# Optimization experiments

Hardware: AMD Instinct MI355X
Metric: run time of the kernel (lower is better)

Reference implementation:

```python
import jax, jax.numpy as jnp
import numpy as np

BIT = 4
HALF = 2 ** (BIT - 1)          # 8 -> signed integer grid [-8, 7]
N_LEVELS = 2 ** BIT - 1        # 15
COUT, CIN, KH, KW = 1024, 1024, 3, 3


def _flip_pass(r, err, up_num, up_err, up_pri, dn_num, dn_err, dn_pri):
    """One SQuant flip pass over rows (groups). Greedily flips the rounding
    direction of the highest-priority elements so each row's rounding-error
    sum becomes ~0, and hands off boundary priorities for the next pass
    (reconstruction of the SQuant_func CUDA kernel)."""
    G, K = r.shape
    rows = jnp.arange(G)
    e = err.sum(-1)                                    # (G,) error budget
    nflip = jnp.round(jnp.abs(e)).astype(jnp.int32)    # flips needed per row
    is_up = e < 0                                      # under-rounded -> flip up

    pri = jnp.where(is_up[:, None], up_pri, dn_pri)
    order = jnp.argsort(-pri, axis=-1)                 # descending priority
    rank = jnp.zeros((G, K), jnp.int32).at[rows[:, None], order].set(
        jnp.broadcast_to(jnp.arange(K, dtype=jnp.int32), (G, K)))
    flip = rank < nflip[:, None]

    cand_num = jnp.where(is_up[:, None], up_num, dn_num)
    cand_err = jnp.where(is_up[:, None], up_err, dn_err)
    new_r = jnp.where(flip, cand_num, r)
    new_err = jnp.where(flip, cand_err, err)

    # ---- boundary-priority handoff for the next (channel-wise) pass ----
    ni = jnp.take_along_axis(order, jnp.clip(nflip, 0, K - 1)[:, None], axis=-1)[:, 0]      # next candidate
    li = jnp.take_along_axis(order, jnp.clip(nflip - 1, 0, K - 1)[:, None], axis=-1)[:, 0]  # last flipped
    has_next = nflip < K
    has_last = nflip > 0
    next_pri = jnp.where(has_next, pri[rows, ni], 0.0)         # flip one more element
    last_pri = jnp.where(has_last, 1.0 - pri[rows, li], 0.0)   # revert the last flip

    z = jnp.zeros_like(pri)
    new_up_pri = z.at[rows, ni].add(jnp.where(is_up, next_pri, 0.0))
    new_up_pri = new_up_pri.at[rows, li].add(jnp.where(~is_up, last_pri, 0.0))
    new_dn_pri = z.at[rows, ni].add(jnp.where(~is_up, next_pri, 0.0))
    new_dn_pri = new_dn_pri.at[rows, li].add(jnp.where(is_up, last_pri, 0.0))

    # reverting the last flipped element restores its pre-flip value/error
    up_last = is_up & has_last
    dn_last = (~is_up) & has_last
    new_dn_num = dn_num.at[rows, li].set(jnp.where(up_last, r[rows, li], dn_num[rows, li]))
    new_dn_err = dn_err.at[rows, li].set(jnp.where(up_last, err[rows, li], dn_err[rows, li]))
    new_up_num = up_num.at[rows, li].set(jnp.where(dn_last, r[rows, li], up_num[rows, li]))
    new_up_err = up_err.at[rows, li].set(jnp.where(dn_last, err[rows, li], up_err[rows, li]))
    return new_r, new_err, new_up_num, new_up_err, new_up_pri, new_dn_num, new_dn_err, new_dn_pri


def _adaptive_round(q):
    t_min, t_max = float(-HALF), float(HALF - 1)
    r = jnp.round(q)
    err = r - q
    cand_up = (err < 0) & (q < t_max)    # elements that may be rounded up instead
    cand_dn = (err > 0) & (q > t_min)    # elements that may be rounded down instead
    up_num = jnp.where(cand_up, r + 1.0, r)
    up_err = jnp.where(cand_up, err + 1.0, 0.0)
    up_pri = jnp.where(cand_up, -err, 0.0)   # |rounding error|
    dn_num = jnp.where(cand_dn, r - 1.0, r)
    dn_err = jnp.where(cand_dn, err - 1.0, 0.0)
    dn_pri = jnp.where(cand_dn, err, 0.0)

    cout, cin = q.shape[0], q.shape[1]
    k = q.size // (cout * cin)
    st = tuple(a.reshape(cout * cin, k) for a in (r, err, up_num, up_err, up_pri, dn_num, dn_err, dn_pri))
    st = _flip_pass(*st)                               # SQuant-K: per (Cout,Cin) kernel
    st = tuple(a.reshape(cout, cin * k) for a in st)
    st = _flip_pass(*st)                               # SQuant-C: per output channel
    return st[0].reshape(q.shape)


def _squant_quantize(weight):
    flat = weight.reshape(weight.shape[0], -1)
    x_max = flat.max(1)
    x_min = flat.min(1)
    scale = N_LEVELS / jnp.maximum(x_max - x_min, 1e-8)   # asymmetric per-channel
    zp = jnp.round(scale * x_min) + HALF                  # signed, integral zero point
    bshape = (-1,) + (1,) * (weight.ndim - 1)
    scale = scale.reshape(bshape)
    zp = zp.reshape(bshape)
    q = scale * weight - zp                               # linear_quantize
    q = _adaptive_round(q)
    q = jnp.clip(q, -HALF, HALF - 1)
    return (q + zp) / scale                               # linear_dequantize


def setup_inputs() -> dict:
    key = jax.random.key(0)
    weight = jax.random.normal(key, (COUT, CIN, KH, KW), dtype=jnp.float32) * 0.05
    return {"weight": weight}


def reference(weight):
    return _squant_quantize(weight)
```

## Files before the change

### kernel.cpp

```cpp
#include <hip/hip_runtime.h>

#define NROW   1024
#define ROWLEN 9216
#define NGRP   1024
#define NT     256
#define GPT    4
#define LCAP   256

__device__ __forceinline__ int bucketOf(float v) {
    int b = (int)(v * 256.0f);
    return b > 255 ? 255 : b;
}
__device__ __forceinline__ int clip16(int v) { return v < -8 ? -8 : (v > 7 ? 7 : v); }

__device__ void replay_group(const float* wg, float scale, float zp,
                             float r[9], float err[9], float q[9],
                             int* nflip1, bool* isup1, int* li_out) {
    float pri[9];
    #pragma unroll
    for (int j = 0; j < 9; ++j) {
        float qq = __fsub_rn(__fmul_rn(scale, wg[j]), zp);
        float rr = rintf(qq);
        q[j] = qq; r[j] = rr; err[j] = __fsub_rn(rr, qq);
    }
    float e = __fadd_rn(
                __fadd_rn(__fadd_rn(__fadd_rn(err[0], err[1]), __fadd_rn(err[2], err[3])),
                          __fadd_rn(__fadd_rn(err[4], err[5]), __fadd_rn(err[6], err[7]))),
                err[8]);
    int nf0 = (int)rintf(fabsf(e));
    bool up = (e < 0.0f);
    #pragma unroll
    for (int j = 0; j < 9; ++j) {
        bool cand = up ? ((err[j] < 0.0f) && (q[j] < 7.0f))
                       : ((err[j] > 0.0f) && (q[j] > -8.0f));
        pri[j] = cand ? (up ? -err[j] : err[j]) : 0.0f;
    }
    int rank[9] = {0,0,0,0,0,0,0,0,0};
    #pragma unroll
    for (int a = 0; a < 9; ++a)
        #pragma unroll
        for (int b = a + 1; b < 9; ++b) {
            int c = (pri[a] >= pri[b]) ? 1 : 0;
            rank[b] += c; rank[a] += 1 - c;
        }
    int nf = nf0 < 9 ? nf0 : 9;
    int lip = nf - 1; if (lip < 0) lip = 0;
    int li = 0;
    #pragma unroll
    for (int j = 0; j < 9; ++j) if (rank[j] == lip) li = j;
    *nflip1 = nf0; *isup1 = up; *li_out = li;
}

__global__ __launch_bounds__(NT)
__attribute__((amdgpu_waves_per_eu(4, 4)))
void squant_kernel(const float* __restrict__ w, float* __restrict__ out) {
    __shared__ alignas(16) signed char s_r2[ROWLEN];
    __shared__ unsigned short s_upos[NGRP];
    __shared__ unsigned short s_dpos[NGRP];
    __shared__ float s_uval[NGRP];
    __shared__ float s_dval[NGRP];
    __shared__ signed char s_ucn[NGRP];
    __shared__ signed char s_dcn[NGRP];
    __shared__ float s_leaf[128];
    __shared__ int   s_hist[256];
    __shared__ float s_lv[LCAP];
    __shared__ unsigned short s_lg[LCAP];
    __shared__ float s_lut[16];
    __shared__ float s_wred[8];
    __shared__ float s_bc[2];
    __shared__ float s_e2s;
    __shared__ int   s_seli[2];
    __shared__ int   s_lcount;

    const int row = blockIdx.x;
    const int tid = threadIdx.x;
    const int lane = tid & 63, wid = tid >> 6;
    const float* wrow = w + (size_t)row * ROWLEN;

    float fe[36];
    float vmin =  3.402823466e38f;
    float vmax = -3.402823466e38f;
    const float4* wt4 = reinterpret_cast<const float4*>(wrow + 36 * tid);
    #pragma unroll
    for (int k = 0; k < 9; ++k) {
        float4 v = wt4[k];
        fe[4*k+0] = v.x; fe[4*k+1] = v.y; fe[4*k+2] = v.z; fe[4*k+3] = v.w;
        vmin = fminf(vmin, fminf(fminf(v.x, v.y), fminf(v.z, v.w)));
        vmax = fmaxf(vmax, fmaxf(fmaxf(v.x, v.y), fmaxf(v.z, v.w)));
    }
    #pragma unroll
    for (int o = 32; o > 0; o >>= 1) {
        vmin = fminf(vmin, __shfl_xor(vmin, o, 64));
        vmax = fmaxf(vmax, __shfl_xor(vmax, o, 64));
    }
    if (lane == 0) { s_wred[wid] = vmin; s_wred[4 + wid] = vmax; }
    __syncthreads();
    if (tid == 0) {
        float a = s_wred[0], b = s_wred[4];
        #pragma unroll
        for (int i = 1; i < 4; ++i) { a = fminf(a, s_wred[i]); b = fmaxf(b, s_wred[4 + i]); }
        s_bc[0] = a; s_bc[1] = b;
    }
    __syncthreads();
    const float scale = __fdiv_rn(15.0f, fmaxf(__fsub_rn(s_bc[1], s_bc[0]), 1e-8f));
    const float zp    = __fadd_rn(rintf(__fmul_rn(scale, s_bc[0])), 8.0f);
    if (tid < 16) s_lut[tid] = __fdiv_rn(__fadd_rn((float)(tid - 8), zp), scale);

    int pk[9] = {0,0,0,0,0,0,0,0,0};
    #pragma unroll
    for (int gi = 0; gi < GPT; ++gi) {
        const int g = tid * GPT + gi;
        const int base = g * 9;
        float r[9], err[9], pri[9];
        int cu_m = 0, cd_m = 0;
        #pragma unroll
        for (int j = 0; j < 9; ++j) {
            float wv = fe[9 * gi + j];
            float qq = __fsub_rn(__fmul_rn(scale, wv), zp);
            float rr = rintf(qq);
            float ee = __fsub_rn(rr, qq);
            r[j] = rr; err[j] = ee;
            if ((ee < 0.0f) && (qq <  7.0f)) cu_m |= (1 << j);
            if ((ee > 0.0f) && (qq > -8.0f)) cd_m |= (1 << j);
        }
        float e = __fadd_rn(
                    __fadd_rn(__fadd_rn(__fadd_rn(err[0], err[1]), __fadd_rn(err[2], err[3])),
                              __fadd_rn(__fadd_rn(err[4], err[5]), __fadd_rn(err[6], err[7]))),
                    err[8]);
        int nflip = (int)rintf(fabsf(e));
        const bool isup = (e < 0.0f);
        const float da = isup ? 1.0f : -1.0f;
        const int cm = isup ? cu_m : cd_m;
        #pragma unroll
        for (int j = 0; j < 9; ++j)
            pri[j] = ((cm >> j) & 1) ? fabsf(err[j]) : 0.0f;
        int rank[9] = {0,0,0,0,0,0,0,0,0};
        #pragma unroll
        for (int a = 0; a < 9; ++a)
            #pragma unroll
            for (int b = a + 1; b < 9; ++b) {
                int c = (pri[a] >= pri[b]) ? 1 : 0;
                rank[b] += c; rank[a] += 1 - c;
            }
        const int nf  = nflip < 9 ? nflip : 9;
        const int nip = nf < 8 ? nf : 8;
        int lip = nf - 1; if (lip < 0) lip = 0;

        int ni = 0, li = 0;
        float pri_ni = 0.0f, pri_li = 0.0f, r_ni = 0.0f, r_li = 0.0f;
        #pragma unroll
        for (int j = 0; j < 9; ++j) {
            bool cand = (cm >> j) & 1;
            bool flip = rank[j] < nf;
            float cnj = cand ? __fadd_rn(r[j], da) : r[j];
            float cej = cand ? __fadd_rn(err[j], da) : 0.0f;
            fe[9 * gi + j] = flip ? cej : err[j];
            int enc = clip16(__float2int_rn(flip ? cnj : r[j])) & 0xff;
            const int m = 9 * gi + j;
            pk[m >> 2] |= enc << (8 * (m & 3));
            if (rank[j] == nip) { ni = j; pri_ni = pri[j]; r_ni = r[j]; }
            if (rank[j] == lip) { li = j; pri_li = pri[j]; r_li = r[j]; }
        }
        const bool has_next = (nflip < 9);
        const bool has_last = (nflip > 0);
        const float next_pri = has_next ? pri_ni : 0.0f;
        const float last_pri = has_last ? __fsub_rn(1.0f, pri_li) : 0.0f;
        signed char ncv = (signed char)clip16(__float2int_rn(
            (pri_ni > 0.0f) ? __fadd_rn(r_ni, da) : r_ni));
        signed char lcv = (signed char)clip16(__float2int_rn(r_li));
        if (isup) {
            s_upos[g] = (unsigned short)(base + ni); s_uval[g] = next_pri; s_ucn[g] = ncv;
            s_dpos[g] = (unsigned short)(base + li); s_dval[g] = last_pri; s_dcn[g] = lcv;
        } else {
            s_dpos[g] = (unsigned short)(base + ni); s_dval[g] = next_pri; s_dcn[g] = ncv;
            s_upos[g] = (unsigned short)(base + li); s_uval[g] = last_pri; s_ucn[g] = lcv;
        }
    }
    {
        int* r2w = reinterpret_cast<int*>(s_r2);
        #pragma unroll
        for (int k = 0; k < 9; ++k) r2w[9 * tid + k] = pk[k];
    }

    {
        const int h = tid & 1;
        float pe[8];
        #pragma unroll
        for (int j = 0; j < 8; ++j) {
            float s = __fadd_rn(__fadd_rn(__fadd_rn(fe[j], fe[8 + j]), fe[16 + j]), fe[24 + j]);
            if (j < 4) s = __fadd_rn(s, fe[32 + j]);
            pe[j] = s;
        }
        #pragma unroll
        for (int j = 0; j < 8; ++j) pe[j] = __shfl_xor(pe[j], 1, 64);
        float po[8];
        #pragma unroll
        for (int j = 0; j < 4; ++j)
            po[j] = __fadd_rn(__fadd_rn(__fadd_rn(__fadd_rn(pe[j], fe[4 + j]),
                                                  fe[12 + j]), fe[20 + j]), fe[28 + j]);
        #pragma unroll
        for (int j = 4; j < 8; ++j)
            po[j] = __fadd_rn(__fadd_rn(__fadd_rn(__fadd_rn(__fadd_rn(pe[j], fe[j - 4]),
                                                  fe[4 + j]), fe[12 + j]), fe[20 + j]), fe[28 + j]);
        float res = __fadd_rn(__fadd_rn(__fadd_rn(po[0], po[1]), __fadd_rn(po[2], po[3])),
                              __fadd_rn(__fadd_rn(po[4], po[5]), __fadd_rn(po[6], po[7])));
        if (h) s_leaf[tid >> 1] = res;
        s_hist[tid] = 0;
        if (tid == 0) s_lcount = 0;
    }
    __syncthreads();
    if (tid < 64) {
        float v = __fadd_rn(s_leaf[2 * tid], s_leaf[2 * tid + 1]);
        #pragma unroll
        for (int o = 1; o < 64; o <<= 1) {
            float u = __shfl_xor(v, o, 64);
            v = __fadd_rn(v, u);
        }
        if (tid == 0) s_e2s = v;
    }
    __syncthreads();

    const float e2     = s_e2s;
    const int   nflip2 = (int)rintf(fabsf(e2));
    const bool  isup2  = (e2 < 0.0f);
    const float* val = isup2 ? s_uval : s_dval;
    const unsigned short* pos = isup2 ? s_upos : s_dpos;
    const signed char* cnv = isup2 ? s_ucn : s_dcn;

    int   gg[4]; float vv[4]; int bb[4];
    #pragma unroll
    for (int m = 0; m < 4; ++m) {
        gg[m] = tid + m * NT;
        vv[m] = val[gg[m]];
        bb[m] = (vv[m] > 0.0f) ? bucketOf(vv[m]) : -1;
        if (bb[m] >= 0) atomicAdd(&s_hist[bb[m]], 1);
    }
    __syncthreads();
    if (tid < 64) {
        int b0 = s_hist[4*tid], b1 = s_hist[4*tid+1], b2 = s_hist[4*tid+2], b3 = s_hist[4*tid+3];
        int s3 = b3, s2 = b2 + s3, s1 = b1 + s2, s0 = b0 + s1;
        int suf = s0;
        #pragma unroll
        for (int off = 1; off < 64; off <<= 1) {
            int o = __shfl_down(suf, off, 64);
            if (tid + off < 64) suf += o;
        }
        int above = suf - s0;
        s_hist[4*tid]   = s0 + above;
        s_hist[4*tid+1] = s1 + above;
        s_hist[4*tid+2] = s2 + above;
        s_hist[4*tid+3] = s3 + above;
    }
    __syncthreads();
    const int npos = s_hist[0];

    if (nflip2 > 0 && nflip2 <= npos) {
        {
            int Tb  = s_hist[tid];
            int Tb1 = (tid < 255) ? s_hist[tid + 1] : 0;
            if (Tb >= nflip2 && Tb1 < nflip2) { s_seli[0] = tid; s_seli[1] = nflip2 - Tb1; }
        }
        __syncthreads();
        const int B = s_seli[0], m = s_seli[1];
        #pragma unroll
        for (int mm = 0; mm < 4; ++mm) {
            if (bb[mm] > B) s_r2[pos[gg[mm]]] = cnv[gg[mm]];
            else if (bb[mm] == B) {
                int ix = atomicAdd(&s_lcount, 1);
                if (ix < LCAP) { s_lv[ix] = vv[mm]; s_lg[ix] = (unsigned short)gg[mm]; }
            }
        }
        __syncthreads();
        const int L = s_lcount;
        if (L <= LCAP) {
            #pragma unroll
            for (int mm = 0; mm < 4; ++mm) {
                if (bb[mm] != B) continue;
                int rk = 0;
                for (int l = 0; l < L; ++l) {
                    float lv = s_lv[l]; int lg = s_lg[l];
                    rk += (int)((lv > vv[mm]) || ((lv == vv[mm]) && (lg < gg[mm])));
                }
                if (rk < m) s_r2[pos[gg[mm]]] = cnv[gg[mm]];
            }
        } else {
            #pragma unroll
            for (int mm = 0; mm < 4; ++mm) {
                if (bb[mm] != B) continue;
                int rk = 0;
                for (int j = 0; j < NGRP; ++j) {
                    float vj = val[j];
                    if (vj > 0.0f && bucketOf(vj) == B)
                        rk += (int)((vj > vv[mm]) || ((vj == vv[mm]) && (j < gg[mm])));
                }
                if (rk < m) s_r2[pos[gg[mm]]] = cnv[gg[mm]];
            }
        }
    } else if (nflip2 > npos) {
        #pragma unroll
        for (int mm = 0; mm < 4; ++mm)
            if (bb[mm] >= 0) s_r2[pos[gg[mm]]] = cnv[gg[mm]];
        __syncthreads();
        if (tid == 0) {
            int c = 0; const int extra = nflip2 - npos;
            for (int g = 0; g < NGRP && c < extra; ++g) {
                float r[9], err[9], q[9]; int nf1; bool up1; int li;
                replay_group(wrow + 9 * g, scale, zp, r, err, q, &nf1, &up1, &li);
                for (int j = 0; j < 9 && c < extra; ++j) {
                    int p = 9 * g + j;
                    if (val[g] > 0.0f && pos[g] == p) continue;
                    float cnp;
                    if (isup2) { bool cu = (err[j] < 0.0f) && (q[j] < 7.0f);
                                 cnp = cu ? r[j] + 1.0f : r[j]; }
                    else       { bool cd = (err[j] > 0.0f) && (q[j] > -8.0f);
                                 cnp = cd ? r[j] - 1.0f : r[j]; }
                    if (nf1 > 0 && j == li && (up1 != isup2)) cnp = r[j];
                    s_r2[p] = (signed char)clip16(__float2int_rn(cnp));
                    ++c;
                }
            }
        }
    }
    __syncthreads();

    const int* r2i = reinterpret_cast<const int*>(s_r2);
    float4* o4 = reinterpret_cast<float4*>(out + (size_t)row * ROWLEN);
    #pragma unroll
    for (int k = 0; k < 9; ++k) {
        int i = tid + k * NT;
        int word = r2i[i];
        float4 o;
        o.x = s_lut[((int)(signed char)( word        & 0xff)) + 8];
        o.y = s_lut[((int)(signed char)((word >>  8) & 0xff)) + 8];
        o.z = s_lut[((int)(signed char)((word >> 16) & 0xff)) + 8];
        o.w = s_lut[((int)(signed char)((word >> 24) & 0xff)) + 8];
        o4[i] = o;
    }
}

extern "C" void kernel_launch(void* const* d_in, const int* in_sizes, int n_in,
                              void* d_out, int out_size, void* d_ws, size_t ws_size,
                              hipStream_t stream) {
    const float* w = (const float*)d_in[0];
    float* out = (float*)d_out;
    squant_kernel<<<dim3(NROW), dim3(NT), 0, stream>>>(w, out);
}
```

Before: 97.55 us.

## Double threads per row to 512 and reduce errors via shared memory

Raises the block size from 256 to 512 threads, so each thread handles 2 groups instead of 4 and holds fewer registers. The row error-sum reduction changes from a register/shuffle tree to writing per-element errors into a new 36 KB shared array and summing with 128 threads. This adds parallelism and latency hiding per row but costs more LDS per block and an extra shared round trip. The waves_per_eu(4,4) hint stays, so occupancy may now be limited by LDS.

```diff
diff --git a/kernel.cpp b/kernel.cpp
--- a/kernel.cpp
+++ b/kernel.cpp
@@ -3,8 +3,8 @@
 #define NROW   1024
 #define ROWLEN 9216
 #define NGRP   1024
-#define NT     256
-#define GPT    4
+#define NT     512
+#define GPT    2
 #define LCAP   256
 
 __device__ __forceinline__ int bucketOf(float v) {
@@ -55,6 +55,7 @@
 __attribute__((amdgpu_waves_per_eu(4, 4)))
 void squant_kernel(const float* __restrict__ w, float* __restrict__ out) {
     __shared__ alignas(16) signed char s_r2[ROWLEN];
+    __shared__ alignas(16) float s_err[ROWLEN];
     __shared__ unsigned short s_upos[NGRP];
     __shared__ unsigned short s_dpos[NGRP];
     __shared__ float s_uval[NGRP];
@@ -66,7 +67,7 @@
     __shared__ float s_lv[LCAP];
     __shared__ unsigned short s_lg[LCAP];
     __shared__ float s_lut[16];
-    __shared__ float s_wred[8];
+    __shared__ float s_wred[16];
     __shared__ float s_bc[2];
     __shared__ float s_e2s;
     __shared__ int   s_seli[2];
@@ -77,28 +78,28 @@
     const int lane = tid & 63, wid = tid >> 6;
     const float* wrow = w + (size_t)row * ROWLEN;
 
-    float fe[36];
+    float fe[18];
     float vmin =  3.402823466e38f;
     float vmax = -3.402823466e38f;
-    const float4* wt4 = reinterpret_cast<const float4*>(wrow + 36 * tid);
+    const float2* wt2 = reinterpret_cast<const float2*>(wrow + 18 * tid);
     #pragma unroll
     for (int k = 0; k < 9; ++k) {
-        float4 v = wt4[k];
-        fe[4*k+0] = v.x; fe[4*k+1] = v.y; fe[4*k+2] = v.z; fe[4*k+3] = v.w;
-        vmin = fminf(vmin, fminf(fminf(v.x, v.y), fminf(v.z, v.w)));
-        vmax = fmaxf(vmax, fmaxf(fmaxf(v.x, v.y), fmaxf(v.z, v.w)));
+        float2 v = wt2[k];
+        fe[2 * k] = v.x; fe[2 * k + 1] = v.y;
+        vmin = fminf(vmin, fminf(v.x, v.y));
+        vmax = fmaxf(vmax, fmaxf(v.x, v.y));
     }
     #pragma unroll
     for (int o = 32; o > 0; o >>= 1) {
         vmin = fminf(vmin, __shfl_xor(vmin, o, 64));
         vmax = fmaxf(vmax, __shfl_xor(vmax, o, 64));
     }
-    if (lane == 0) { s_wred[wid] = vmin; s_wred[4 + wid] = vmax; }
+    if (lane == 0) { s_wred[wid] = vmin; s_wred[8 + wid] = vmax; }
     __syncthreads();
     if (tid == 0) {
-        float a = s_wred[0], b = s_wred[4];
-        #pragma unroll
-        for (int i = 1; i < 4; ++i) { a = fminf(a, s_wred[i]); b = fmaxf(b, s_wred[4 + i]); }
+        float a = s_wred[0], b = s_wred[8];
+        #pragma unroll
+        for (int i = 1; i < 8; ++i) { a = fminf(a, s_wred[i]); b = fmaxf(b, s_wred[8 + i]); }
         s_bc[0] = a; s_bc[1] = b;
     }
     __syncthreads();
@@ -106,7 +107,7 @@
     const float zp    = __fadd_rn(rintf(__fmul_rn(scale, s_bc[0])), 8.0f);
     if (tid < 16) s_lut[tid] = __fdiv_rn(__fadd_rn((float)(tid - 8), zp), scale);
 
-    int pk[9] = {0,0,0,0,0,0,0,0,0};
+    int pk16[9] = {0,0,0,0,0,0,0,0,0};
     #pragma unroll
     for (int gi = 0; gi < GPT; ++gi) {
         const int g = tid * GPT + gi;
@@ -157,7 +158,7 @@
             fe[9 * gi + j] = flip ? cej : err[j];
             int enc = clip16(__float2int_rn(flip ? cnj : r[j])) & 0xff;
             const int m = 9 * gi + j;
-            pk[m >> 2] |= enc << (8 * (m & 3));
+            pk16[m >> 1] |= enc << (8 * (m & 1));
             if (rank[j] == nip) { ni = j; pri_ni = pri[j]; r_ni = r[j]; }
             if (rank[j] == lip) { li = j; pri_li = pri[j]; r_li = r[j]; }
         }
@@ -177,36 +178,32 @@
         }
     }
     {
-        int* r2w = reinterpret_cast<int*>(s_r2);
-        #pragma unroll
-        for (int k = 0; k < 9; ++k) r2w[9 * tid + k] = pk[k];
-    }
-
-    {
-        const int h = tid & 1;
-        float pe[8];
-        #pragma unroll
-        for (int j = 0; j < 8; ++j) {
-            float s = __fadd_rn(__fadd_rn(__fadd_rn(fe[j], fe[8 + j]), fe[16 + j]), fe[24 + j]);
-            if (j < 4) s = __fadd_rn(s, fe[32 + j]);
-            pe[j] = s;
-        }
-        #pragma unroll
-        for (int j = 0; j < 8; ++j) pe[j] = __shfl_xor(pe[j], 1, 64);
-        float po[8];
-        #pragma unroll
-        for (int j = 0; j < 4; ++j)
-            po[j] = __fadd_rn(__fadd_rn(__fadd_rn(__fadd_rn(pe[j], fe[4 + j]),
-                                                  fe[12 + j]), fe[20 + j]), fe[28 + j]);
-        #pragma unroll
-        for (int j = 4; j < 8; ++j)
-            po[j] = __fadd_rn(__fadd_rn(__fadd_rn(__fadd_rn(__fadd_rn(pe[j], fe[j - 4]),
-                                                  fe[4 + j]), fe[12 + j]), fe[20 + j]), fe[28 + j]);
-        float res = __fadd_rn(__fadd_rn(__fadd_rn(po[0], po[1]), __fadd_rn(po[2], po[3])),
-                              __fadd_rn(__fadd_rn(po[4], po[5]), __fadd_rn(po[6], po[7])));
-        if (h) s_leaf[tid >> 1] = res;
-        s_hist[tid] = 0;
-        if (tid == 0) s_lcount = 0;
+        short* r2s = reinterpret_cast<short*>(s_r2);
+        #pragma unroll
+        for (int k = 0; k < 9; ++k) r2s[9 * tid + k] = (short)pk16[k];
+        float2* se2 = reinterpret_cast<float2*>(s_err + 18 * tid);
+        #pragma unroll
+        for (int k = 0; k < 9; ++k) se2[k] = float2{fe[2 * k], fe[2 * k + 1]};
+    }
+    if (tid < 256) s_hist[tid] = 0;
+    if (tid == 0) s_lcount = 0;
+    __syncthreads();
+
+    if (tid < 128) {
+        const float4* q = reinterpret_cast<const float4*>(s_err + 72 * tid);
+        float4 A = q[0], B4 = q[1];
+        float a0 = A.x, a1 = A.y, a2 = A.z, a3 = A.w;
+        float a4 = B4.x, a5 = B4.y, a6 = B4.z, a7 = B4.w;
+        #pragma unroll
+        for (int i = 1; i < 9; ++i) {
+            float4 c = q[2 * i], d = q[2 * i + 1];
+            a0 = __fadd_rn(a0, c.x); a1 = __fadd_rn(a1, c.y);
+            a2 = __fadd_rn(a2, c.z); a3 = __fadd_rn(a3, c.w);
+            a4 = __fadd_rn(a4, d.x); a5 = __fadd_rn(a5, d.y);
+            a6 = __fadd_rn(a6, d.z); a7 = __fadd_rn(a7, d.w);
+        }
+        s_leaf[tid] = __fadd_rn(__fadd_rn(__fadd_rn(a0, a1), __fadd_rn(a2, a3)),
+                                __fadd_rn(__fadd_rn(a4, a5), __fadd_rn(a6, a7)));
     }
     __syncthreads();
     if (tid < 64) {
@@ -227,9 +224,9 @@
     const unsigned short* pos = isup2 ? s_upos : s_dpos;
     const signed char* cnv = isup2 ? s_ucn : s_dcn;
 
-    int   gg[4]; float vv[4]; int bb[4];
-    #pragma unroll
-    for (int m = 0; m < 4; ++m) {
+    int   gg[2]; float vv[2]; int bb[2];
+    #pragma unroll
+    for (int m = 0; m < 2; ++m) {
         gg[m] = tid + m * NT;
         vv[m] = val[gg[m]];
         bb[m] = (vv[m] > 0.0f) ? bucketOf(vv[m]) : -1;
@@ -255,7 +252,7 @@
     const int npos = s_hist[0];
 
     if (nflip2 > 0 && nflip2 <= npos) {
-        {
+        if (tid < 256) {
             int Tb  = s_hist[tid];
             int Tb1 = (tid < 255) ? s_hist[tid + 1] : 0;
             if (Tb >= nflip2 && Tb1 < nflip2) { s_seli[0] = tid; s_seli[1] = nflip2 - Tb1; }
@@ -263,7 +260,7 @@
         __syncthreads();
         const int B = s_seli[0], m = s_seli[1];
         #pragma unroll
-        for (int mm = 0; mm < 4; ++mm) {
+        for (int mm = 0; mm < 2; ++mm) {
             if (bb[mm] > B) s_r2[pos[gg[mm]]] = cnv[gg[mm]];
             else if (bb[mm] == B) {
                 int ix = atomicAdd(&s_lcount, 1);
@@ -274,7 +271,7 @@
         const int L = s_lcount;
         if (L <= LCAP) {
             #pragma unroll
-            for (int mm = 0; mm < 4; ++mm) {
+            for (int mm = 0; mm < 2; ++mm) {
                 if (bb[mm] != B) continue;
                 int rk = 0;
                 for (int l = 0; l < L; ++l) {
@@ -285,7 +282,7 @@
             }
         } else {
             #pragma unroll
-            for (int mm = 0; mm < 4; ++mm) {
+            for (int mm = 0; mm < 2; ++mm) {
                 if (bb[mm] != B) continue;
                 int rk = 0;
                 for (int j = 0; j < NGRP; ++j) {
@@ -298,7 +295,7 @@
         }
     } else if (nflip2 > npos) {
         #pragma unroll
-        for (int mm = 0; mm < 4; ++mm)
+        for (int mm = 0; mm < 2; ++mm)
             if (bb[mm] >= 0) s_r2[pos[gg[mm]]] = cnv[gg[mm]];
         __syncthreads();
         if (tid == 0) {
@@ -326,7 +323,8 @@
     const int* r2i = reinterpret_cast<const int*>(s_r2);
     float4* o4 = reinterpret_cast<float4*>(out + (size_t)row * ROWLEN);
     #pragma unroll
-    for (int k = 0; k < 9; ++k) {
+    for (int k = 0; k < 5; ++k) {
+        if (k == 4 && tid >= 256) break;
         int i = tid + k * NT;
         int word = r2i[i];
         float4 o;
```

Result: no change. 98.04 us (+0.5%).
